# Optimization experiments

Hardware: AMD Instinct MI355X
Metric: run time of the kernel (lower is better)

Reference implementation:

```python
import jax, jax.numpy as jnp
import numpy as np

M = 2048      # mention groups (spans with antecedents)
K_MAX = 128   # max antecedents per mention
N = 4096      # candidate span pool
G = 1000      # span representation dim
D = 20        # distance/genre/speaker embed dim
H = 150       # Score MLP hidden
GIJ = 3 * G + 3 * D  # 3060


def setup_inputs() -> dict:
    key = jax.random.key(0)
    ks = jax.random.split(key, 12)
    # ragged group lengths (deterministic): cycle 1..K_MAX, sum = P = 132096
    lengths = np.tile(np.arange(1, K_MAX + 1), M // K_MAX).astype(np.int32)
    P = int(lengths.sum())
    seg_ids = np.repeat(np.arange(M), lengths).astype(np.int32)
    starts = np.cumsum(lengths) - lengths
    offsets = (np.arange(P) - starts[seg_ids]).astype(np.int32)

    genre_emb = jax.random.normal(ks[3], (8, D), jnp.float32) * 0.02
    genre_emb = genre_emb.at[0].set(0.0)   # padding_idx=0
    speaker_emb = jax.random.normal(ks[4], (3, D), jnp.float32) * 0.02
    speaker_emb = speaker_emb.at[0].set(0.0)  # padding_idx=0

    return {
        "g_i": jax.random.normal(ks[0], (N, G), jnp.float32),
        "mention_scores": jax.random.normal(ks[1], (N, 1), jnp.float32),
        "dist_emb": jax.random.normal(ks[2], (9, D), jnp.float32) * 0.02,
        "genre_emb": genre_emb,
        "speaker_emb": speaker_emb,
        "W1": jax.random.normal(ks[5], (GIJ, H), jnp.float32) / np.sqrt(GIJ),
        "b1": jnp.zeros((H,), jnp.float32),
        "W2": jax.random.normal(ks[6], (H, H), jnp.float32) / np.sqrt(H),
        "b2": jnp.zeros((H,), jnp.float32),
        "W3": jax.random.normal(ks[7], (H, 1), jnp.float32) / np.sqrt(H),
        "b3": jnp.zeros((1,), jnp.float32),
        "mention_ids": jax.random.randint(ks[8], (P,), 0, N, jnp.int32),
        "antecedent_ids": jax.random.randint(ks[9], (P,), 0, N, jnp.int32),
        "dist_ids": jax.random.randint(ks[10], (P,), 0, 9, jnp.int32),
        "genre_ids": jax.random.randint(ks[11], (P,), 0, 8, jnp.int32),
        "speaker_ids": jax.random.randint(jax.random.fold_in(key, 99), (P,), 0, 3, jnp.int32),
        "lengths": jnp.asarray(lengths),
        "seg_ids": jnp.asarray(seg_ids),
        "offsets": jnp.asarray(offsets),
    }


def reference(g_i, mention_scores, dist_emb, genre_emb, speaker_emb,
              W1, b1, W2, b2, W3, b3,
              mention_ids, antecedent_ids, dist_ids, genre_ids, speaker_ids,
              lengths, seg_ids, offsets):
    # feature gathers: phi = [distance, genre, speaker] embeddings, (P, 3D)
    phi = jnp.concatenate(
        [dist_emb[dist_ids], genre_emb[genre_ids], speaker_emb[speaker_ids]], axis=1)
    i_g = g_i[mention_ids]      # (P, G)
    j_g = g_i[antecedent_ids]   # (P, G)
    pairs = jnp.concatenate([i_g, j_g, i_g * j_g, phi], axis=1)  # (P, GIJ)

    # 3-layer scoring MLP (dropout inactive at eval)
    h = jax.nn.relu(pairs @ W1 + b1)
    h = jax.nn.relu(h @ W2 + b2)
    s_ij = (h @ W3 + b3)[:, 0]  # (P,)

    scores = mention_scores[mention_ids, 0] + mention_scores[antecedent_ids, 0] + s_ij

    # per-group softmax over [group scores, epsilon=0] via segment ops
    seg_max = jax.ops.segment_max(scores, seg_ids, num_segments=M)
    m = jnp.maximum(seg_max, 0.0)                      # include epsilon 0
    e = jnp.exp(scores - m[seg_ids])                   # (P,)
    eps_e = jnp.exp(-m)                                # (M,)
    denom = jax.ops.segment_sum(e, seg_ids, num_segments=M) + eps_e
    pair_probs = e / denom[seg_ids]                    # (P,)
    eps_probs = eps_e / denom                          # (M,)

    # pad_and_stack(value=1000): row 0 is the empty leading group -> [1, 1000...]
    grid = jnp.full((M + 1, K_MAX + 1), 1000.0, dtype=scores.dtype)
    grid = grid.at[seg_ids + 1, offsets].set(pair_probs)
    grid = grid.at[jnp.arange(M) + 1, lengths].set(eps_probs)
    grid = grid.at[0, 0].set(1.0)
    return grid
```

## Files before the change

### kernel.cpp

```cpp
#include <hip/hip_runtime.h>

#define P_TOTAL 132096
#define NPOOL   4096
#define GDIM    1000
#define HDIM    150
#define MGRP    2048
#define KMAX    128

typedef __attribute__((ext_vector_type(4))) float f32x4;
typedef __attribute__((ext_vector_type(2))) float f32x2;
typedef __attribute__((ext_vector_type(4))) unsigned int u32x4;

#define OFF_W1C8   0
#define OFF_W1AB8  163840
#define OFF_W2F8   491520
#define OFF_ABPRE  517120
#define OFF_TABS   3138560
#define OFF_SGRID  3151360
#define OFF_GF8    4200448
#define OFF_EXTRAS 8394752

__device__ __forceinline__ short f2bf(float f) {
  union { float f; unsigned u; } v; v.f = f;
  unsigned r = v.u + 0x7FFFu + ((v.u >> 16) & 1u);
  return (short)(r >> 16);
}
__device__ __forceinline__ float bf2f(unsigned short s) {
  return __builtin_bit_cast(float, ((unsigned)s) << 16);
}
__device__ __forceinline__ unsigned char f2fp8(float f) {
  int d = __builtin_amdgcn_cvt_pk_fp8_f32(f, 0.f, 0, false);
  return (unsigned char)(d & 0xFF);
}
__device__ __forceinline__ long mk64(unsigned lo, unsigned hi) {
  return (long)(((unsigned long long)hi << 32) | lo);
}

__device__ __forceinline__ u32x4 fp8prod16(u32x4 m, u32x4 a) {
  u32x4 r;
  #pragma unroll
  for (int d = 0; d < 4; ++d) {
    f32x2 ml = __builtin_amdgcn_cvt_pk_f32_fp8(m[d], false);
    f32x2 mh = __builtin_amdgcn_cvt_pk_f32_fp8(m[d], true);
    f32x2 al = __builtin_amdgcn_cvt_pk_f32_fp8(a[d], false);
    f32x2 ah = __builtin_amdgcn_cvt_pk_f32_fp8(a[d], true);
    f32x2 pl = ml * al, ph = mh * ah;
    int o = __builtin_amdgcn_cvt_pk_fp8_f32(pl[0], pl[1], 0, false);
    o = __builtin_amdgcn_cvt_pk_fp8_f32(ph[0], ph[1], o, true);
    r[d] = (unsigned)o;
  }
  return r;
}

#define T1 (32*160*32)
#define T2 (32*320*32)
#define T3 (5*160*32)
#define TF (NPOOL*256)
#define TT (20*160)
__global__ __launch_bounds__(256) void prep_kernel(
    const float* __restrict__ W1, const float* __restrict__ W2,
    const float* __restrict__ g_i,
    const float* __restrict__ dist_emb, const float* __restrict__ genre_emb,
    const float* __restrict__ spk_emb, const float* __restrict__ b1,
    unsigned char* __restrict__ w1c8, unsigned char* __restrict__ w1ab8,
    unsigned char* __restrict__ w2f8, unsigned* __restrict__ gf8,
    float* __restrict__ tabs) {
  int idx = blockIdx.x * 256 + threadIdx.x;
  if (idx < T1) {
    int c = idx / (160*32); int rem = idx % (160*32);
    int n = rem / 32, kk = rem % 32;
    int s = c >> 1, j = c & 1;
    int g = kk >> 3, i = kk & 7;
    int q = g ^ ((n >> 2) & 3);
    int k = s*64 + q*16 + j*8 + i;
    float v = (k < GDIM && n < HDIM) ? W1[(2000 + k)*HDIM + n] : 0.f;
    w1c8[idx] = f2fp8(v);
  } else if (idx < T1 + T2) {
    int i = idx - T1;
    int c = i / (320*32); int rem = i % (320*32);
    int n = rem / 32, kk = rem % 32;
    int s = c >> 2, j = c & 3;
    int k = s*128 + (kk >> 3)*32 + j*8 + (kk & 7);
    float v = 0.f;
    if (k < GDIM) {
      if (n < HDIM)                 v = W1[k*HDIM + n];
      else if (n >= 160 && n < 310) v = W1[(1000 + k)*HDIM + (n - 160)];
    }
    w1ab8[i] = f2fp8(v);
  } else if (idx < T1 + T2 + T3) {
    int i = idx - T1 - T2;
    int c = i / (160*32); int rem = i % (160*32);
    int n = rem / 32, kk = rem % 32;
    int g = kk >> 3, ii = kk & 7;
    int q = g ^ ((n >> 2) & 3);
    int k = c*32 + q*8 + ii;
    float v = (k < HDIM && n < HDIM) ? W2[k*HDIM + n] : 0.f;
    w2f8[i] = f2fp8(v);
  } else if (idx < T1 + T2 + T3 + TF) {
    int i = idx - T1 - T2 - T3;
    int row = i >> 8, jd = i & 255;
    int c0 = jd * 4;
    float f0 = (c0     < GDIM) ? g_i[row*GDIM + c0]     : 0.f;
    float f1 = (c0 + 1 < GDIM) ? g_i[row*GDIM + c0 + 1] : 0.f;
    float f2 = (c0 + 2 < GDIM) ? g_i[row*GDIM + c0 + 2] : 0.f;
    float f3 = (c0 + 3 < GDIM) ? g_i[row*GDIM + c0 + 3] : 0.f;
    int d = 0;
    d = __builtin_amdgcn_cvt_pk_fp8_f32(f0, f1, d, false);
    d = __builtin_amdgcn_cvt_pk_fp8_f32(f2, f3, d, true);
    gf8[i] = (unsigned)d;
  } else if (idx < T1 + T2 + T3 + TF + TT) {
    int i = idx - T1 - T2 - T3 - TF;
    int row = i / 160, n = i % 160;
    float acc = 0.f;
    if (n < HDIM) {
      const float* emb; int woff;
      if (row < 9)       { emb = dist_emb  + row*20;      woff = 3000; acc = b1[n]; }
      else if (row < 17) { emb = genre_emb + (row-9)*20;  woff = 3020; }
      else               { emb = spk_emb   + (row-17)*20; woff = 3040; }
      #pragma unroll
      for (int kk = 0; kk < 20; ++kk) acc += emb[kk] * W1[(woff + kk)*HDIM + n];
    }
    tabs[i] = acc;
  }
}

__global__ __launch_bounds__(256) void pre_gemm_kernel(
    const unsigned char* __restrict__ gf8, const unsigned char* __restrict__ w1ab8,
    unsigned short* __restrict__ abpre) {
  int wave = threadIdx.x >> 6, lane = threadIdx.x & 63;
  int quad = lane >> 4, n16 = lane & 15;
  int rowbase = blockIdx.x * 64 + wave * 16;
  int colbase = blockIdx.y * 80;

  f32x4 acc[5];
  #pragma unroll
  for (int t = 0; t < 5; ++t) acc[t] = (f32x4){0.f, 0.f, 0.f, 0.f};

  const unsigned char* arow = gf8 + (long)(rowbase + n16) * 1024 + quad*32;

  for (int s = 0; s < 8; ++s) {
    u32x4 Aa = *(const u32x4*)(arow + s*128);
    u32x4 Ab = *(const u32x4*)(arow + s*128 + 16);
    #pragma unroll
    for (int j = 0; j < 4; ++j) {
      long a = (j == 0) ? mk64(Aa[0], Aa[1]) : (j == 1) ? mk64(Aa[2], Aa[3])
             : (j == 2) ? mk64(Ab[0], Ab[1]) : mk64(Ab[2], Ab[3]);
      const unsigned char* bp = w1ab8 + (((s*4 + j)*320 + colbase + n16) * 32 + quad*8);
      #pragma unroll
      for (int t = 0; t < 5; ++t) {
        long b = *(const long*)(bp + t*16*32);
        acc[t] = __builtin_amdgcn_mfma_f32_16x16x32_fp8_fp8(a, b, acc[t], 0, 0, 0);
      }
    }
  }
  #pragma unroll
  for (int t = 0; t < 5; ++t) {
    #pragma unroll
    for (int r = 0; r < 4; ++r) {
      int row = rowbase + quad*4 + r;
      abpre[(long)row * 320 + colbase + t*16 + n16] = (unsigned short)f2bf(acc[t][r]);
    }
  }
}

__global__ __launch_bounds__(256) void extras_kernel(
    const unsigned short* __restrict__ abpre, const float* __restrict__ tabs,
    const int* __restrict__ mid, const int* __restrict__ aid,
    const int* __restrict__ did, const int* __restrict__ gid,
    const int* __restrict__ sid,
    unsigned short* __restrict__ extras, int pbase) {
  int t = threadIdx.x;
  int lp = blockIdx.x * 8 + (t >> 5);
  int p = pbase + lp;
  int l = t & 31;
  int m = mid[p], a = aid[p];
  const float* Dd = tabs + did[p]*160;
  const float* Ge = tabs + (9 + gid[p])*160;
  const float* Se = tabs + (17 + sid[p])*160;
  #pragma unroll
  for (int j = 0; j < 5; ++j) {
    int n = l + j*32;
    float v = bf2f(abpre[(long)m*320 + n]) + bf2f(abpre[(long)a*320 + 160 + n])
            + Dd[n] + Ge[n] + Se[n];
    extras[(long)lp*160 + n] = (unsigned short)f2bf(v);
  }
}

__global__ __launch_bounds__(256) void mlp_kernel(
    const unsigned char* __restrict__ gf8,
    const unsigned short* __restrict__ extras,
    const unsigned char* __restrict__ w1c8,
    const unsigned char* __restrict__ w2f8,
    const float* __restrict__ ms,
    const float* __restrict__ W3, const float* __restrict__ b2,
    const float* __restrict__ b3,
    const int* __restrict__ mention_ids, const int* __restrict__ antecedent_ids,
    const int* __restrict__ seg_ids, const int* __restrict__ offs,
    float* __restrict__ sgrid, int pbase) {

  __shared__ __align__(16) unsigned char lds[53248];

  int tid = threadIdx.x;
  int wave = tid >> 6, lane = tid & 63;
  int quad = lane >> 4, n16 = lane & 15;
  int lp0 = blockIdx.x * 128;
  int gp0 = pbase + lp0;
  int wrow = wave * 32;

  int jj = (lane & 3) ^ ((lane >> 2) & 3) ^ ((lane >> 4) & 1);
  int srow = lane >> 2;
  int swA = quad ^ (n16 & 3) ^ ((n16 >> 2) & 1);
  int swB = quad ^ ((n16 >> 2) & 3);

  const unsigned char* pA0 =
      gf8 + (long)mention_ids[gp0 + wave*16 + srow] * 1024 + jj*16;
  const unsigned char* pA1 =
      gf8 + (long)mention_ids[gp0 + (wave + 4)*16 + srow] * 1024 + jj*16;
  const unsigned char* pA2 =
      gf8 + (long)antecedent_ids[gp0 + wave*16 + srow] * 1024 + jj*16;
  const unsigned char* pA3 =
      gf8 + (long)antecedent_ids[gp0 + (wave + 4)*16 + srow] * 1024 + jj*16;
  int dA0 = wave*1024,      dA1 = (wave + 4)*1024;
  int dA2 = 8192 + dA0,     dA3 = 8192 + dA1;

  f32x4 acc0[10], acc1[10];
  #pragma unroll
  for (int t = 0; t < 10; ++t) {
    acc0[t] = (f32x4){0.f, 0.f, 0.f, 0.f};
    acc1[t] = (f32x4){0.f, 0.f, 0.f, 0.f};
  }

  auto issue = [&](int s, int buf) {
    unsigned char* base = lds + buf*26624;
    long so = (long)s * 64;
    __builtin_amdgcn_global_load_lds((const unsigned int*)(pA0 + so),
        (unsigned int*)(base + dA0 + lane*16), 16, 0, 0);
    __builtin_amdgcn_global_load_lds((const unsigned int*)(pA1 + so),
        (unsigned int*)(base + dA1 + lane*16), 16, 0, 0);
    __builtin_amdgcn_global_load_lds((const unsigned int*)(pA2 + so),
        (unsigned int*)(base + dA2 + lane*16), 16, 0, 0);
    __builtin_amdgcn_global_load_lds((const unsigned int*)(pA3 + so),
        (unsigned int*)(base + dA3 + lane*16), 16, 0, 0);
    const unsigned char* wsrc = w1c8 + (long)s*10240;
    __builtin_amdgcn_global_load_lds((const unsigned int*)(wsrc + wave*1024 + (long)lane*16),
        (unsigned int*)(base + 16384 + wave*1024 + lane*16), 16, 0, 0);
    __builtin_amdgcn_global_load_lds((const unsigned int*)(wsrc + (wave+4)*1024 + (long)lane*16),
        (unsigned int*)(base + 16384 + (wave+4)*1024 + lane*16), 16, 0, 0);
    if (wave < 2)
      __builtin_amdgcn_global_load_lds((const unsigned int*)(wsrc + (wave+8)*1024 + (long)lane*16),
          (unsigned int*)(base + 16384 + (wave+8)*1024 + lane*16), 16, 0, 0);
  };

  issue(0, 0);
  for (int s = 0; s < 16; ++s) {
    __syncthreads();
    if (s < 15) issue(s + 1, (s + 1) & 1);
    const unsigned char* cb = lds + (s & 1)*26624;

    u32x4 M0 = *(const u32x4*)(cb + (wrow + n16)*64 + swA*16);
    u32x4 C0 = *(const u32x4*)(cb + 8192 + (wrow + n16)*64 + swA*16);
    u32x4 M1 = *(const u32x4*)(cb + (wrow + 16 + n16)*64 + swA*16);
    u32x4 C1 = *(const u32x4*)(cb + 8192 + (wrow + 16 + n16)*64 + swA*16);
    u32x4 P0 = fp8prod16(M0, C0);
    u32x4 P1 = fp8prod16(M1, C1);

    #pragma unroll
    for (int j = 0; j < 2; ++j) {
      long a0 = (j == 0) ? mk64(P0[0], P0[1]) : mk64(P0[2], P0[3]);
      long a1 = (j == 0) ? mk64(P1[0], P1[1]) : mk64(P1[2], P1[3]);
      const unsigned char* bp = cb + 16384 + j*5120 + n16*32 + swB*8;
      #pragma unroll
      for (int t = 0; t < 10; ++t) {
        long b = *(const long*)(bp + t*512);
        acc0[t] = __builtin_amdgcn_mfma_f32_16x16x32_fp8_fp8(a0, b, acc0[t], 0, 0, 0);
        acc1[t] = __builtin_amdgcn_mfma_f32_16x16x32_fp8_fp8(a1, b, acc1[t], 0, 0, 0);
      }
    }
  }
  __syncthreads();

  for (int r = wave; r < 25; r += 4) {
    __builtin_amdgcn_global_load_lds(
        (const unsigned int*)(w2f8 + r*1024 + (long)lane*16),
        (unsigned int*)(lds + 26624 + r*1024), 16, 0, 0);
  }

  unsigned char* h1w = lds + wave * 5888;
  #pragma unroll
  for (int t = 0; t < 10; ++t) {
    int n = t*16 + n16;
    #pragma unroll
    for (int r = 0; r < 4; ++r) {
      int row0 = quad*4 + r;
      float v0 = acc0[t][r] + bf2f(extras[(long)(lp0 + wrow + row0)*160 + n]);
      float v1 = acc1[t][r] + bf2f(extras[(long)(lp0 + wrow + 16 + row0)*160 + n]);
      h1w[row0*184 + n]        = f2fp8(fmaxf(v0, 0.f));
      h1w[(16 + row0)*184 + n] = f2fp8(fmaxf(v1, 0.f));
    }
  }
  __syncthreads();

  float bias3 = b3[0];
  float w3v[10], b2v[10];
  #pragma unroll
  for (int t = 0; t < 10; ++t) {
    int n = t*16 + n16;
    w3v[t] = (n < HDIM) ? W3[n] : 0.f;
    b2v[t] = (n < HDIM) ? b2[n] : 0.f;
  }

  #pragma unroll
  for (int tile = 0; tile < 2; ++tile) {
    f32x4 acc2[10];
    #pragma unroll
    for (int t = 0; t < 10; ++t) acc2[t] = (f32x4){0.f, 0.f, 0.f, 0.f};

    #pragma unroll
    for (int c = 0; c < 5; ++c) {
      long a = *(const long*)(h1w + (tile*16 + n16)*184 + c*32 + quad*8);
      const unsigned char* bp = lds + 26624 + (c*160 + n16)*32 + swB*8;
      #pragma unroll
      for (int t = 0; t < 10; ++t) {
        long b = *(const long*)(bp + t*512);
        acc2[t] = __builtin_amdgcn_mfma_f32_16x16x32_fp8_fp8(a, b, acc2[t], 0, 0, 0);
      }
    }

    float part[4] = {0.f, 0.f, 0.f, 0.f};
    #pragma unroll
    for (int t = 0; t < 10; ++t) {
      #pragma unroll
      for (int r = 0; r < 4; ++r) {
        float h2 = fmaxf(acc2[t][r] + b2v[t], 0.f);
        part[r] += h2 * w3v[t];
      }
    }
    for (int msk = 1; msk < 16; msk <<= 1) {
      #pragma unroll
      for (int r = 0; r < 4; ++r) part[r] += __shfl_xor(part[r], msk);
    }

    if (n16 == 0) {
      #pragma unroll
      for (int r = 0; r < 4; ++r) {
        int gp = gp0 + wrow + tile*16 + quad*4 + r;
        float sc = part[r] + bias3 + ms[mention_ids[gp]] + ms[antecedent_ids[gp]];
        sgrid[seg_ids[gp] * KMAX + offs[gp]] = sc;
      }
    }
  }
}

__global__ __launch_bounds__(128) void softmax_kernel(const float* __restrict__ sgrid,
                                                      const int* __restrict__ lengths,
                                                      float* __restrict__ out) {
  int b = blockIdx.x, t = threadIdx.x;
  if (b == 0) {
    out[t] = (t == 0) ? 1.0f : 1000.0f;
    if (t == 0) out[128] = 1000.0f;
    return;
  }
  int m = b - 1;
  int len = lengths[m];
  float s = (t < len) ? sgrid[m * KMAX + t] : -1e30f;

  __shared__ float redA[2];
  __shared__ float redB[2];

  float v = s;
  #pragma unroll
  for (int o = 32; o >= 1; o >>= 1) v = fmaxf(v, __shfl_xor(v, o));
  if ((t & 63) == 0) redA[t >> 6] = v;
  __syncthreads();
  float mx = fmaxf(fmaxf(redA[0], redA[1]), 0.0f);

  float e = (t < len) ? expf(s - mx) : 0.f;
  float sum = e;
  #pragma unroll
  for (int o = 32; o >= 1; o >>= 1) sum += __shfl_xor(sum, o);
  if ((t & 63) == 0) redB[t >> 6] = sum;
  __syncthreads();

  float eps_e = expf(-mx);
  float denom = redB[0] + redB[1] + eps_e;

  float* row = out + (long)(m + 1) * 129;
  float val;
  if (t < len)       val = e / denom;
  else if (t == len) val = eps_e / denom;
  else               val = 1000.0f;
  row[t] = val;
  if (t == 0) row[128] = (len == KMAX) ? (eps_e / denom) : 1000.0f;
}

extern "C" void kernel_launch(void* const* d_in, const int* in_sizes, int n_in,
                              void* d_out, int out_size, void* d_ws, size_t ws_size,
                              hipStream_t stream) {
  const float* g_i        = (const float*)d_in[0];
  const float* ms         = (const float*)d_in[1];
  const float* dist_emb   = (const float*)d_in[2];
  const float* genre_emb  = (const float*)d_in[3];
  const float* spk_emb    = (const float*)d_in[4];
  const float* W1         = (const float*)d_in[5];
  const float* b1         = (const float*)d_in[6];
  const float* W2         = (const float*)d_in[7];
  const float* b2         = (const float*)d_in[8];
  const float* W3         = (const float*)d_in[9];
  const float* b3         = (const float*)d_in[10];
  const int* mention_ids    = (const int*)d_in[11];
  const int* antecedent_ids = (const int*)d_in[12];
  const int* dist_ids       = (const int*)d_in[13];
  const int* genre_ids      = (const int*)d_in[14];
  const int* spk_ids        = (const int*)d_in[15];
  const int* lengths        = (const int*)d_in[16];
  const int* seg_ids        = (const int*)d_in[17];
  const int* offsets        = (const int*)d_in[18];

  char* ws = (char*)d_ws;
  unsigned char* w1c8  = (unsigned char*)(ws + OFF_W1C8);
  unsigned char* w1ab8 = (unsigned char*)(ws + OFF_W1AB8);
  unsigned char* w2f8  = (unsigned char*)(ws + OFF_W2F8);
  unsigned short* abpre = (unsigned short*)(ws + OFF_ABPRE);
  float* tabs   = (float*)(ws + OFF_TABS);
  float* sgrid  = (float*)(ws + OFF_SGRID);
  unsigned char* gf8  = (unsigned char*)(ws + OFF_GF8);
  unsigned short* extras = (unsigned short*)(ws + OFF_EXTRAS);

  size_t avail = (ws_size > OFF_EXTRAS) ? ws_size - OFF_EXTRAS : 0;
  int nchunk;
  if      (avail >= (size_t)P_TOTAL * 320)      nchunk = 1;
  else if (avail >= (size_t)P_TOTAL * 160)      nchunk = 2;
  else if (avail >= (size_t)P_TOTAL * 80)       nchunk = 4;
  else                                          nchunk = 8;
  int npc = P_TOTAL / nchunk;

  const int prepN = T1 + T2 + T3 + TF + TT;
  prep_kernel<<<(prepN + 255)/256, 256, 0, stream>>>(W1, W2, g_i,
                                                     dist_emb, genre_emb, spk_emb, b1,
                                                     w1c8, w1ab8, w2f8,
                                                     (unsigned*)gf8, tabs);
  dim3 gpre(NPOOL/64, 4);
  pre_gemm_kernel<<<gpre, 256, 0, stream>>>(gf8, w1ab8, abpre);
  for (int c = 0; c < nchunk; ++c) {
    int pbase = c * npc;
    extras_kernel<<<npc/8, 256, 0, stream>>>(abpre, tabs,
                                             mention_ids, antecedent_ids,
                                             dist_ids, genre_ids, spk_ids,
                                             extras, pbase);
    mlp_kernel<<<npc/128, 256, 0, stream>>>(gf8, extras, w1c8, w2f8, ms,
                                            W3, b2, b3,
                                            mention_ids, antecedent_ids,
                                            seg_ids, offsets, sgrid, pbase);
  }
  softmax_kernel<<<MGRP + 1, 128, 0, stream>>>(sgrid, lengths, (float*)d_out);
}
```

Measured before the change: 204.8 us.

## Fuse extras gather into MLP epilogue and precombine embedding tables

Removes the separate extras kernel and its P×160 bf16 intermediate buffer. The MLP layer-1 epilogue now gathers the precomputed mention/antecedent projections directly from abpre. It also reads a single combined dist×genre×speaker table (216 rows, with b1 folded in) that prep_kernel builds. This cuts a global write/read round trip and extra launches, at the cost of more scattered gathers inside the MLP kernel.

```diff
diff --git a/kernel.cpp b/kernel.cpp
--- a/kernel.cpp
+++ b/kernel.cpp
@@ -15,10 +15,9 @@
 #define OFF_W1AB8  163840
 #define OFF_W2F8   491520
 #define OFF_ABPRE  517120
-#define OFF_TABS   3138560
-#define OFF_SGRID  3151360
-#define OFF_GF8    4200448
-#define OFF_EXTRAS 8394752
+#define OFF_TABS2  3138560
+#define OFF_SGRID  3276800
+#define OFF_GF8    4325376
 
 __device__ __forceinline__ short f2bf(float f) {
   union { float f; unsigned u; } v; v.f = f;
@@ -56,7 +55,7 @@
 #define T2 (32*320*32)
 #define T3 (5*160*32)
 #define TF (NPOOL*256)
-#define TT (20*160)
+#define TT (216*160)
 __global__ __launch_bounds__(256) void prep_kernel(
     const float* __restrict__ W1, const float* __restrict__ W2,
     const float* __restrict__ g_i,
@@ -64,7 +63,7 @@
     const float* __restrict__ spk_emb, const float* __restrict__ b1,
     unsigned char* __restrict__ w1c8, unsigned char* __restrict__ w1ab8,
     unsigned char* __restrict__ w2f8, unsigned* __restrict__ gf8,
-    float* __restrict__ tabs) {
+    float* __restrict__ tabs2) {
   int idx = blockIdx.x * 256 + threadIdx.x;
   if (idx < T1) {
     int c = idx / (160*32); int rem = idx % (160*32);
@@ -113,14 +112,16 @@
     int row = i / 160, n = i % 160;
     float acc = 0.f;
     if (n < HDIM) {
-      const float* emb; int woff;
-      if (row < 9)       { emb = dist_emb  + row*20;      woff = 3000; acc = b1[n]; }
-      else if (row < 17) { emb = genre_emb + (row-9)*20;  woff = 3020; }
-      else               { emb = spk_emb   + (row-17)*20; woff = 3040; }
-      #pragma unroll
-      for (int kk = 0; kk < 20; ++kk) acc += emb[kk] * W1[(woff + kk)*HDIM + n];
-    }
-    tabs[i] = acc;
+      int d = row / 24, g = (row / 3) % 8, sp = row % 3;
+      acc = b1[n];
+      #pragma unroll
+      for (int kk = 0; kk < 20; ++kk) {
+        acc += dist_emb [d*20 + kk]  * W1[(3000 + kk)*HDIM + n];
+        acc += genre_emb[g*20 + kk]  * W1[(3020 + kk)*HDIM + n];
+        acc += spk_emb  [sp*20 + kk] * W1[(3040 + kk)*HDIM + n];
+      }
+    }
+    tabs2[i] = acc;
   }
 }
 
@@ -163,48 +164,27 @@
   }
 }
 
-__global__ __launch_bounds__(256) void extras_kernel(
-    const unsigned short* __restrict__ abpre, const float* __restrict__ tabs,
-    const int* __restrict__ mid, const int* __restrict__ aid,
-    const int* __restrict__ did, const int* __restrict__ gid,
-    const int* __restrict__ sid,
-    unsigned short* __restrict__ extras, int pbase) {
-  int t = threadIdx.x;
-  int lp = blockIdx.x * 8 + (t >> 5);
-  int p = pbase + lp;
-  int l = t & 31;
-  int m = mid[p], a = aid[p];
-  const float* Dd = tabs + did[p]*160;
-  const float* Ge = tabs + (9 + gid[p])*160;
-  const float* Se = tabs + (17 + sid[p])*160;
-  #pragma unroll
-  for (int j = 0; j < 5; ++j) {
-    int n = l + j*32;
-    float v = bf2f(abpre[(long)m*320 + n]) + bf2f(abpre[(long)a*320 + 160 + n])
-            + Dd[n] + Ge[n] + Se[n];
-    extras[(long)lp*160 + n] = (unsigned short)f2bf(v);
-  }
-}
-
 __global__ __launch_bounds__(256) void mlp_kernel(
     const unsigned char* __restrict__ gf8,
-    const unsigned short* __restrict__ extras,
+    const unsigned short* __restrict__ abpre,
+    const float* __restrict__ tabs2,
     const unsigned char* __restrict__ w1c8,
     const unsigned char* __restrict__ w2f8,
     const float* __restrict__ ms,
     const float* __restrict__ W3, const float* __restrict__ b2,
     const float* __restrict__ b3,
     const int* __restrict__ mention_ids, const int* __restrict__ antecedent_ids,
+    const int* __restrict__ dist_ids, const int* __restrict__ genre_ids,
+    const int* __restrict__ spk_ids,
     const int* __restrict__ seg_ids, const int* __restrict__ offs,
-    float* __restrict__ sgrid, int pbase) {
+    float* __restrict__ sgrid) {
 
   __shared__ __align__(16) unsigned char lds[53248];
 
   int tid = threadIdx.x;
   int wave = tid >> 6, lane = tid & 63;
   int quad = lane >> 4, n16 = lane & 15;
-  int lp0 = blockIdx.x * 128;
-  int gp0 = pbase + lp0;
+  int gp0 = blockIdx.x * 128;
   int wrow = wave * 32;
 
   int jj = (lane & 3) ^ ((lane >> 2) & 3) ^ ((lane >> 4) & 1);
@@ -287,15 +267,27 @@
 
   unsigned char* h1w = lds + wave * 5888;
   #pragma unroll
-  for (int t = 0; t < 10; ++t) {
-    int n = t*16 + n16;
+  for (int tile = 0; tile < 2; ++tile) {
+    int idm[4], ida[4], itab[4];
     #pragma unroll
     for (int r = 0; r < 4; ++r) {
-      int row0 = quad*4 + r;
-      float v0 = acc0[t][r] + bf2f(extras[(long)(lp0 + wrow + row0)*160 + n]);
-      float v1 = acc1[t][r] + bf2f(extras[(long)(lp0 + wrow + 16 + row0)*160 + n]);
-      h1w[row0*184 + n]        = f2fp8(fmaxf(v0, 0.f));
-      h1w[(16 + row0)*184 + n] = f2fp8(fmaxf(v1, 0.f));
+      int gp = gp0 + wrow + tile*16 + quad*4 + r;
+      idm[r]  = mention_ids[gp];
+      ida[r]  = antecedent_ids[gp];
+      itab[r] = dist_ids[gp]*24 + genre_ids[gp]*3 + spk_ids[gp];
+    }
+    f32x4* acc = tile ? acc1 : acc0;
+    #pragma unroll
+    for (int t = 0; t < 10; ++t) {
+      int n = t*16 + n16;
+      #pragma unroll
+      for (int r = 0; r < 4; ++r) {
+        float v = acc[t][r]
+                + bf2f(abpre[(long)idm[r]*320 + n])
+                + bf2f(abpre[(long)ida[r]*320 + 160 + n])
+                + tabs2[itab[r]*160 + n];
+        h1w[(tile*16 + quad*4 + r)*184 + n] = f2fp8(fmaxf(v, 0.f));
+      }
     }
   }
   __syncthreads();
@@ -421,36 +413,21 @@
   unsigned char* w1ab8 = (unsigned char*)(ws + OFF_W1AB8);
   unsigned char* w2f8  = (unsigned char*)(ws + OFF_W2F8);
   unsigned short* abpre = (unsigned short*)(ws + OFF_ABPRE);
-  float* tabs   = (float*)(ws + OFF_TABS);
+  float* tabs2  = (float*)(ws + OFF_TABS2);
   float* sgrid  = (float*)(ws + OFF_SGRID);
   unsigned char* gf8  = (unsigned char*)(ws + OFF_GF8);
-  unsigned short* extras = (unsigned short*)(ws + OFF_EXTRAS);
-
-  size_t avail = (ws_size > OFF_EXTRAS) ? ws_size - OFF_EXTRAS : 0;
-  int nchunk;
-  if      (avail >= (size_t)P_TOTAL * 320)      nchunk = 1;
-  else if (avail >= (size_t)P_TOTAL * 160)      nchunk = 2;
-  else if (avail >= (size_t)P_TOTAL * 80)       nchunk = 4;
-  else                                          nchunk = 8;
-  int npc = P_TOTAL / nchunk;
 
   const int prepN = T1 + T2 + T3 + TF + TT;
   prep_kernel<<<(prepN + 255)/256, 256, 0, stream>>>(W1, W2, g_i,
                                                      dist_emb, genre_emb, spk_emb, b1,
                                                      w1c8, w1ab8, w2f8,
-                                                     (unsigned*)gf8, tabs);
+                                                     (unsigned*)gf8, tabs2);
   dim3 gpre(NPOOL/64, 4);
   pre_gemm_kernel<<<gpre, 256, 0, stream>>>(gf8, w1ab8, abpre);
-  for (int c = 0; c < nchunk; ++c) {
-    int pbase = c * npc;
-    extras_kernel<<<npc/8, 256, 0, stream>>>(abpre, tabs,
-                                             mention_ids, antecedent_ids,
-                                             dist_ids, genre_ids, spk_ids,
-                                             extras, pbase);
-    mlp_kernel<<<npc/128, 256, 0, stream>>>(gf8, extras, w1c8, w2f8, ms,
-                                            W3, b2, b3,
-                                            mention_ids, antecedent_ids,
-                                            seg_ids, offsets, sgrid, pbase);
-  }
+  mlp_kernel<<<P_TOTAL/128, 256, 0, stream>>>(gf8, abpre, tabs2, w1c8, w2f8, ms,
+                                              W3, b2, b3,
+                                              mention_ids, antecedent_ids,
+                                              dist_ids, genre_ids, spk_ids,
+                                              seg_ids, offsets, sgrid);
   softmax_kernel<<<MGRP + 1, 128, 0, stream>>>(sgrid, lengths, (float*)d_out);
 }
```

Result: slower. 232.8 us (+13.7%).
